# Kernel tuning notes

Measured on AMD Instinct MI355X. Metric: run time of the kernel, lower is better.

The kernel has to match this reference:

```python
import jax, jax.numpy as jnp
import numpy as np

S, D, H, KV, HD = 2048, 4096, 32, 8, 128
N_REP = H // KV
THETA = 50000.0
EPS = 1e-6

# Precompute RoPE tables (constant, matches precompute_freqs_cis sliced to seq_len)
_freqs = 1.0 / THETA ** (np.arange(0, HD, 2)[: HD // 2].astype(np.float32) / HD)
_ang = np.outer(np.arange(S), _freqs).astype(np.float32)  # [S, HD//2]
COS = jnp.asarray(np.cos(_ang))
SIN = jnp.asarray(np.sin(_ang))


def _rope(x):
    # x: [S, nh, HD]; treat last dim as HD//2 complex pairs, multiply by e^{i*ang}
    xr = x.astype(jnp.float32).reshape(S, x.shape[1], HD // 2, 2)
    x0, x1 = xr[..., 0], xr[..., 1]
    c = COS[:, None, :]
    s = SIN[:, None, :]
    o0 = x0 * c - x1 * s
    o1 = x0 * s + x1 * c
    return jnp.stack((o0, o1), axis=-1).reshape(S, x.shape[1], HD)


def setup_inputs() -> dict:
    key = jax.random.key(0)
    k1, k2, k3, k4, k5 = jax.random.split(key, 5)
    w_scale = 0.02
    return {
        "hidden": jax.random.normal(k1, (S, D), dtype=jnp.float32),
        "norm_w": jnp.ones((D,), dtype=jnp.float32),
        "wq": jax.random.normal(k2, (H * HD, D), dtype=jnp.float32) * w_scale,
        "wk": jax.random.normal(k3, (KV * HD, D), dtype=jnp.float32) * w_scale,
        "wv": jax.random.normal(k4, (KV * HD, D), dtype=jnp.float32) * w_scale,
        "wo": jax.random.normal(k5, (D, D), dtype=jnp.float32) * w_scale,
    }


def reference(hidden, norm_w, wq, wk, wv, wo):
    # RMSNorm (per token)
    x = hidden.astype(jnp.float32)
    h = x * jax.lax.rsqrt(jnp.mean(x * x, axis=-1, keepdims=True) + EPS) * norm_w

    # QKV projections (eqx.nn.Linear: y = W @ x, no bias)
    q = (h @ wq.T).reshape(S, H, HD)
    k = (h @ wk.T).reshape(S, KV, HD)
    v = (h @ wv.T).reshape(S, KV, HD)

    # RoPE in fp32 (apply_rotary_emb with dtype=float32)
    q = _rope(q)
    k = _rope(k)

    # GQA: repeat kv heads to match query heads
    k = jnp.repeat(k[:, :, None, :], N_REP, axis=2).reshape(S, H, HD)
    v = jnp.repeat(v[:, :, None, :], N_REP, axis=2).reshape(S, H, HD)

    # Causal attention (full score matrix + softmax, as in the original)
    scores = jnp.einsum("shd,thd->hst", q, k) / jnp.sqrt(jnp.float32(HD))
    mask = jnp.triu(jnp.full((S, S), float("-inf"), dtype=scores.dtype), k=1)
    probs = jax.nn.softmax(scores + mask, axis=-1)
    attn = jnp.einsum("hst,thd->shd", probs, v).reshape(S, H * HD)

    # Output projection
    return attn @ wo.T
```

## Files before the change

### kernel.cpp

```cpp
#include <hip/hip_runtime.h>
#include <stdint.h>
#include <stddef.h>

#define AS1 __attribute__((address_space(1)))
#define AS3 __attribute__((address_space(3)))

typedef short short8 __attribute__((ext_vector_type(8)));
typedef float v4f    __attribute__((ext_vector_type(4)));
typedef unsigned short us4 __attribute__((ext_vector_type(4)));

constexpr int S_  = 2048;
constexpr int D_  = 4096;
constexpr int H_  = 32;
constexpr int KV_ = 8;
constexpr int HD_ = 128;
constexpr int NQKV_ = H_*HD_ + 2*KV_*HD_;
constexpr float SCALE_L2E = 0.12751744154070513f;
constexpr float NLOG2T_64 = -0.24390063241307518f;

__device__ __forceinline__ unsigned short f2bf(float f){
  union { float f; unsigned u; } v; v.f = f;
  unsigned r = v.u + 0x7FFFu + ((v.u >> 16) & 1u);
  return (unsigned short)(r >> 16);
}
__device__ __forceinline__ float bf2f(unsigned short h){
  union { unsigned u; float f; } v; v.u = ((unsigned)h) << 16; return v.f;
}

__device__ __forceinline__ void gl_lds16(const unsigned short* g, unsigned short* l){
  __builtin_amdgcn_global_load_lds((AS1 unsigned int*)(uintptr_t)g,
                                   (AS3 unsigned int*)l, 16, 0, 0);
}

__global__ __launch_bounds__(256) void rmsnorm_k(const float* __restrict__ hidden,
                                                 const float* __restrict__ w,
                                                 unsigned short* __restrict__ out){
  const int s = blockIdx.x, tid = threadIdx.x;
  const float4* row = (const float4*)(hidden + (size_t)s * D_);
  float4 v[4];
  float ss = 0.f;
  #pragma unroll
  for (int i = 0; i < 4; i++){
    float4 t = row[tid + 256*i]; v[i] = t;
    ss += t.x*t.x + t.y*t.y + t.z*t.z + t.w*t.w;
  }
  #pragma unroll
  for (int off = 32; off >= 1; off >>= 1) ss += __shfl_xor(ss, off, 64);
  __shared__ float wsum[4];
  if ((tid & 63) == 0) wsum[tid >> 6] = ss;
  __syncthreads();
  const float total = wsum[0] + wsum[1] + wsum[2] + wsum[3];
  const float r = rsqrtf(total * (1.0f / D_) + 1e-6f);
  const float4* w4 = (const float4*)w;
  us4* o = (us4*)(out + (size_t)s * D_);
  #pragma unroll
  for (int i = 0; i < 4; i++){
    float4 t = v[i], ww = w4[tid + 256*i];
    us4 p;
    p[0] = f2bf(t.x * r * ww.x); p[1] = f2bf(t.y * r * ww.y);
    p[2] = f2bf(t.z * r * ww.z); p[3] = f2bf(t.w * r * ww.w);
    o[tid + 256*i] = p;
  }
}

__global__ __launch_bounds__(256) void cast_k(const float* __restrict__ src,
                                              unsigned short* __restrict__ dst, int n4){
  const int i = blockIdx.x * 256 + threadIdx.x;
  if (i >= n4) return;
  float4 t = ((const float4*)src)[i];
  us4 p;
  p[0] = f2bf(t.x); p[1] = f2bf(t.y); p[2] = f2bf(t.z); p[3] = f2bf(t.w);
  ((us4*)dst)[i] = p;
}

__global__ __launch_bounds__(256) void gemm_bt(const unsigned short* __restrict__ A,
                                               const unsigned short* __restrict__ B,
                                               void* __restrict__ Cp,
                                               int K, int ldc, int f32out){
  __shared__ __align__(16) unsigned short sA[128*32];
  __shared__ __align__(16) unsigned short sB[128*32];
  const int tid = threadIdx.x;
  const int wave = tid >> 6, lane = tid & 63, l15 = lane & 15, quad = lane >> 4;
  const int m0 = blockIdx.y * 128, n0 = blockIdx.x * 128;
  const int wm = wave & 1, wn = wave >> 1;

  v4f acc[4][4];
  #pragma unroll
  for (int i = 0; i < 4; i++)
    #pragma unroll
    for (int j = 0; j < 4; j++) acc[i][j] = (v4f){0.f,0.f,0.f,0.f};

  const int arow = tid >> 2, acol = (tid & 3) * 8;
  const unsigned short* gA = A + (size_t)(m0 + arow) * K + acol;
  const unsigned short* gB = B + (size_t)(n0 + arow) * K + acol;
  unsigned short* lA = sA + wave * 512;
  unsigned short* lB = sB + wave * 512;

  for (int kt = 0; kt < K; kt += 32){
    gl_lds16(gA,                 lA);
    gl_lds16(gA + (size_t)64*K,  lA + 2048);
    gl_lds16(gB,                 lB);
    gl_lds16(gB + (size_t)64*K,  lB + 2048);
    gA += 32; gB += 32;
    __syncthreads();

    short8 af[4], bfr[4];
    #pragma unroll
    for (int mt = 0; mt < 4; mt++)
      af[mt] = *(const short8*)(sA + (wm*64 + mt*16 + l15)*32 + quad*8);
    #pragma unroll
    for (int nt = 0; nt < 4; nt++)
      bfr[nt] = *(const short8*)(sB + (wn*64 + nt*16 + l15)*32 + quad*8);
    #pragma unroll
    for (int mt = 0; mt < 4; mt++)
      #pragma unroll
      for (int nt = 0; nt < 4; nt++)
        acc[mt][nt] = __builtin_amdgcn_mfma_f32_16x16x32_bf16(af[mt], bfr[nt], acc[mt][nt], 0, 0, 0);
    __syncthreads();
  }

  if (f32out){
    float* Cf = (float*)Cp;
    #pragma unroll
    for (int mt = 0; mt < 4; mt++)
      #pragma unroll
      for (int r = 0; r < 4; r++){
        const size_t row = (size_t)(m0 + wm*64 + mt*16 + quad*4 + r);
        float* crow = Cf + row * ldc + n0 + wn*64 + l15;
        #pragma unroll
        for (int nt = 0; nt < 4; nt++) crow[nt*16] = acc[mt][nt][r];
      }
  } else {
    unsigned short* Cb = (unsigned short*)Cp;
    #pragma unroll
    for (int mt = 0; mt < 4; mt++)
      #pragma unroll
      for (int r = 0; r < 4; r++){
        const size_t row = (size_t)(m0 + wm*64 + mt*16 + quad*4 + r);
        unsigned short* crow = Cb + row * ldc + n0 + wn*64 + l15;
        #pragma unroll
        for (int nt = 0; nt < 4; nt++) crow[nt*16] = f2bf(acc[mt][nt][r]);
      }
  }
}

__global__ __launch_bounds__(256) void rope_q_k(const unsigned short* __restrict__ qkv,
                                                unsigned short* __restrict__ qa){
  const int idx = blockIdx.x * 256 + threadIdx.x;
  const int j = idx & 63, h = (idx >> 6) & (H_-1), s = idx >> 11;
  const unsigned pair = *(const unsigned*)(qkv + (size_t)s*NQKV_ + h*HD_ + 2*j);
  const float x0 = bf2f((unsigned short)(pair & 0xffffu));
  const float x1 = bf2f((unsigned short)(pair >> 16));
  const float ang = (float)s * exp2f((float)j * NLOG2T_64);
  const float c = __cosf(ang), sn = __sinf(ang);
  const unsigned o = (unsigned)f2bf((x0*c - x1*sn) * SCALE_L2E)
                   | ((unsigned)f2bf((x0*sn + x1*c) * SCALE_L2E) << 16);
  *(unsigned*)(qa + ((size_t)h*S_ + s)*HD_ + 2*j) = o;
}

__global__ __launch_bounds__(256) void rope_kk(const unsigned short* __restrict__ qkv,
                                               unsigned short* __restrict__ ka){
  const int idx = blockIdx.x * 256 + threadIdx.x;
  const int j = idx & 63, kv = (idx >> 6) & (KV_-1), s = idx >> 9;
  const unsigned pair = *(const unsigned*)(qkv + (size_t)s*NQKV_ + H_*HD_ + kv*HD_ + 2*j);
  const float x0 = bf2f((unsigned short)(pair & 0xffffu));
  const float x1 = bf2f((unsigned short)(pair >> 16));
  const float ang = (float)s * exp2f((float)j * NLOG2T_64);
  const float c = __cosf(ang), sn = __sinf(ang);
  const unsigned o = (unsigned)f2bf(x0*c - x1*sn) | ((unsigned)f2bf(x0*sn + x1*c) << 16);
  *(unsigned*)(ka + ((size_t)kv*S_ + s)*HD_ + 2*j) = o;
}

__global__ __launch_bounds__(256) void vtrans_k(const unsigned short* __restrict__ qkv,
                                                unsigned short* __restrict__ vt){
  const int idx = blockIdx.x * 256 + threadIdx.x;
  const int s = idx & (S_-1), d = (idx >> 11) & (HD_-1), kv = idx >> 18;
  vt[idx] = qkv[(size_t)s*NQKV_ + (H_+KV_)*HD_ + kv*HD_ + d];
}

__device__ __forceinline__ void stage_kv(const unsigned short* __restrict__ ka,
                                         const unsigned short* __restrict__ vt,
                                         unsigned short* sKbuf, unsigned short* sVbuf,
                                         int hk, int t0, int wave, int lane){
  const int l15 = lane & 15, quad = lane >> 4;
  #pragma unroll
  for (int j = 0; j < 4; j++){
    const int c = wave*4 + j;
    const int kt = c >> 2, kk = c & 3;
    gl_lds16(ka + (size_t)(hk*S_ + t0 + kt*16 + l15)*HD_ + kk*32 + quad*8,
             sKbuf + c*512);
  }
  #pragma unroll
  for (int j = 0; j < 4; j++){
    const int c = wave*4 + j;
    const int nt = c >> 1, kk2 = c & 1;
    gl_lds16(vt + (size_t)(hk*HD_ + nt*16 + l15)*S_ + t0 + kk2*32 + quad*8,
             sVbuf + c*512);
  }
}

__global__ __launch_bounds__(256, 2) void attn_k(const unsigned short* __restrict__ qa,
                                                 const unsigned short* __restrict__ ka,
                                                 const unsigned short* __restrict__ vt,
                                                 unsigned short* __restrict__ out){
  const int h = blockIdx.x, p = blockIdx.y;
  const int tid = threadIdx.x, wave = tid >> 6, lane = tid & 63;
  const int l15 = lane & 15, quad = lane >> 4;
  const int hk = h >> 2;
  const int nbB = 32 - p;
  const int total = nbB + p + 1;

  __shared__ __align__(16) unsigned short sK[2][8192];
  __shared__ __align__(16) unsigned short sV[2][8192];
  __shared__ __align__(16) unsigned short sP[4][1024];
  unsigned short* pl = &sP[wave][0];

  short8 ones;
  #pragma unroll
  for (int i = 0; i < 8; i++) ones[i] = (short)0x3F80;

  int tile = 31 - p;
  short8 qf[4];
  {
    const unsigned short* qb = qa + (size_t)(h*S_ + tile*64 + wave*16 + l15)*HD_ + quad*8;
    #pragma unroll
    for (int kk = 0; kk < 4; kk++) qf[kk] = *(const short8*)(qb + kk*32);
  }

  v4f O[8];
  #pragma unroll
  for (int nt = 0; nt < 8; nt++) O[nt] = (v4f){0.f,0.f,0.f,0.f};
  float mrow[4], lrow[4];
  #pragma unroll
  for (int r = 0; r < 4; r++){ mrow[r] = -1e30f; lrow[r] = 0.f; }

  stage_kv(ka, vt, sK[0], sV[0], hk, 0, wave, lane);
  __syncthreads();

  for (int u = 0; u < total; ++u){
    const int cur = u & 1;
    if (u + 1 < total){
      const int b2 = (u + 1 < nbB) ? u + 1 : u + 1 - nbB;
      stage_kv(ka, vt, sK[cur^1], sV[cur^1], hk, b2*64, wave, lane);
    }

    const unsigned short* Kb = &sK[cur][0];
    v4f sc[4];
    #pragma unroll
    for (int kt = 0; kt < 4; kt++) sc[kt] = (v4f){0.f,0.f,0.f,0.f};
    #pragma unroll
    for (int kt = 0; kt < 4; kt++)
      #pragma unroll
      for (int kk = 0; kk < 4; kk++){
        const short8 kf = *(const short8*)(Kb + (kt*4 + kk)*512 + lane*8);
        sc[kt] = __builtin_amdgcn_mfma_f32_16x16x32_bf16(qf[kk], kf, sc[kt], 0, 0, 0);
      }

    const bool diag = (u == nbB - 1) || (u == total - 1);
    float alpha[4];
    #pragma unroll
    for (int r = 0; r < 4; r++){
      float a0 = sc[0][r], a1 = sc[1][r], a2 = sc[2][r], a3 = sc[3][r];
      if (diag){
        const int rloc = wave*16 + quad*4 + r;
        if (     l15 > rloc) a0 = -1e30f;
        if (16 + l15 > rloc) a1 = -1e30f;
        if (32 + l15 > rloc) a2 = -1e30f;
        if (48 + l15 > rloc) a3 = -1e30f;
      }
      float mx = fmaxf(fmaxf(a0, a1), fmaxf(a2, a3));
      #pragma unroll
      for (int off = 1; off < 16; off <<= 1) mx = fmaxf(mx, __shfl_xor(mx, off, 16));
      const float mnew = fmaxf(mrow[r], mx);
      alpha[r] = exp2f(mrow[r] - mnew);
      mrow[r] = mnew;
      const float e0 = exp2f(a0 - mnew);
      const float e1 = exp2f(a1 - mnew);
      const float e2 = exp2f(a2 - mnew);
      const float e3 = exp2f(a3 - mnew);
      const int mr = (quad*4 + r)*8 + (l15 & 7);
      const int hi = (l15 >> 3) * 128;
      pl[      hi       + mr] = f2bf(e0);
      pl[      hi + 256 + mr] = f2bf(e1);
      pl[512 + hi       + mr] = f2bf(e2);
      pl[512 + hi + 256 + mr] = f2bf(e3);
    }
    #pragma unroll
    for (int nt = 0; nt < 8; nt++)
      #pragma unroll
      for (int r = 0; r < 4; r++) O[nt][r] *= alpha[r];

    __builtin_amdgcn_s_waitcnt(0xC07F);
    const short8 pf0 = *(const short8*)(pl + lane*8);
    const short8 pf1 = *(const short8*)(pl + 512 + lane*8);

    v4f rs = (v4f){0.f,0.f,0.f,0.f};
    rs = __builtin_amdgcn_mfma_f32_16x16x32_bf16(pf0, ones, rs, 0, 0, 0);
    rs = __builtin_amdgcn_mfma_f32_16x16x32_bf16(pf1, ones, rs, 0, 0, 0);

    const unsigned short* Vb = &sV[cur][0];
    #pragma unroll
    for (int nt = 0; nt < 8; nt++){
      const short8 vf0 = *(const short8*)(Vb + (nt*2    )*512 + lane*8);
      const short8 vf1 = *(const short8*)(Vb + (nt*2 + 1)*512 + lane*8);
      O[nt] = __builtin_amdgcn_mfma_f32_16x16x32_bf16(pf0, vf0, O[nt], 0, 0, 0);
      O[nt] = __builtin_amdgcn_mfma_f32_16x16x32_bf16(pf1, vf1, O[nt], 0, 0, 0);
    }
    #pragma unroll
    for (int r = 0; r < 4; r++) lrow[r] = lrow[r]*alpha[r] + rs[r];

    __syncthreads();

    if (u == nbB - 1){
      #pragma unroll
      for (int r = 0; r < 4; r++){
        const float inv = 1.0f / lrow[r];
        const size_t row = (size_t)(tile*64 + wave*16 + quad*4 + r);
        #pragma unroll
        for (int nt = 0; nt < 8; nt++)
          out[row*D_ + h*HD_ + nt*16 + l15] = f2bf(O[nt][r] * inv);
      }
      tile = p;
      const unsigned short* qb = qa + (size_t)(h*S_ + tile*64 + wave*16 + l15)*HD_ + quad*8;
      #pragma unroll
      for (int kk = 0; kk < 4; kk++) qf[kk] = *(const short8*)(qb + kk*32);
      #pragma unroll
      for (int nt = 0; nt < 8; nt++) O[nt] = (v4f){0.f,0.f,0.f,0.f};
      #pragma unroll
      for (int r = 0; r < 4; r++){ mrow[r] = -1e30f; lrow[r] = 0.f; }
    }
  }

  #pragma unroll
  for (int r = 0; r < 4; r++){
    const float inv = 1.0f / lrow[r];
    const size_t row = (size_t)(tile*64 + wave*16 + quad*4 + r);
    #pragma unroll
    for (int nt = 0; nt < 8; nt++)
      out[row*D_ + h*HD_ + nt*16 + l15] = f2bf(O[nt][r] * inv);
  }
}

extern "C" void kernel_launch(void* const* d_in, const int* in_sizes, int n_in,
                              void* d_out, int out_size, void* d_ws, size_t ws_size,
                              hipStream_t stream){
  (void)in_sizes; (void)n_in; (void)out_size; (void)ws_size;
  const float* hidden = (const float*)d_in[0];
  const float* norm_w = (const float*)d_in[1];
  const float* wq = (const float*)d_in[2];
  const float* wk = (const float*)d_in[3];
  const float* wv = (const float*)d_in[4];
  const float* wo = (const float*)d_in[5];

  char* ws = (char*)d_ws;
  unsigned short* h_bf  = (unsigned short*)(ws);
  unsigned short* wqkv  = (unsigned short*)(ws + (size_t)(16u) * 1048576u);
  unsigned short* qkv   = (unsigned short*)(ws + (size_t)(64u) * 1048576u);
  unsigned short* qa    = (unsigned short*)(ws + (size_t)(88u) * 1048576u);
  unsigned short* ka    = (unsigned short*)(ws + (size_t)(104u) * 1048576u);
  unsigned short* vt    = (unsigned short*)(ws + (size_t)(108u) * 1048576u);
  unsigned short* wo_bf = (unsigned short*)(ws + (size_t)(16u) * 1048576u);
  unsigned short* attnb = (unsigned short*)(ws + (size_t)(48u) * 1048576u);

  rmsnorm_k<<<S_, 256, 0, stream>>>(hidden, norm_w, h_bf);

  cast_k<<<(D_*D_/4)/256, 256, 0, stream>>>(wq, wqkv, D_*D_/4);
  cast_k<<<(KV_*HD_*D_/4)/256, 256, 0, stream>>>(wk, wqkv + (size_t)H_*HD_*D_, KV_*HD_*D_/4);
  cast_k<<<(KV_*HD_*D_/4)/256, 256, 0, stream>>>(wv, wqkv + (size_t)(H_+KV_)*HD_*D_, KV_*HD_*D_/4);

  gemm_bt<<<dim3(NQKV_/128, S_/128), 256, 0, stream>>>(h_bf, wqkv, qkv, D_, NQKV_, 0);

  rope_q_k<<<(S_*H_*64)/256, 256, 0, stream>>>(qkv, qa);
  rope_kk <<<(S_*KV_*64)/256, 256, 0, stream>>>(qkv, ka);
  vtrans_k<<<(KV_*HD_*S_)/256, 256, 0, stream>>>(qkv, vt);

  cast_k<<<(D_*D_/4)/256, 256, 0, stream>>>(wo, wo_bf, D_*D_/4);

  attn_k<<<dim3(H_, 16), 256, 0, stream>>>(qa, ka, vt, attnb);

  gemm_bt<<<dim3(D_/128, S_/128), 256, 0, stream>>>(attnb, wo_bf, d_out, D_, D_, 1);
}
```

Measured before the change: 556.8 us.

## Fuse RoPE and V transpose into QKV GEMM epilogue, retile attention, split-K output GEMM

```diff
diff --git a/kernel.cpp b/kernel.cpp
--- a/kernel.cpp
+++ b/kernel.cpp
@@ -14,7 +14,6 @@
 constexpr int H_  = 32;
 constexpr int KV_ = 8;
 constexpr int HD_ = 128;
-constexpr int NQKV_ = H_*HD_ + 2*KV_*HD_;
 constexpr float SCALE_L2E = 0.12751744154070513f;
 constexpr float NLOG2T_64 = -0.24390063241307518f;
 
@@ -22,9 +21,6 @@
   union { float f; unsigned u; } v; v.f = f;
   unsigned r = v.u + 0x7FFFu + ((v.u >> 16) & 1u);
   return (unsigned short)(r >> 16);
-}
-__device__ __forceinline__ float bf2f(unsigned short h){
-  union { unsigned u; float f; } v; v.u = ((unsigned)h) << 16; return v.f;
 }
 
 __device__ __forceinline__ void gl_lds16(const unsigned short* g, unsigned short* l){
@@ -73,10 +69,11 @@
   ((us4*)dst)[i] = p;
 }
 
-__global__ __launch_bounds__(256) void gemm_bt(const unsigned short* __restrict__ A,
-                                               const unsigned short* __restrict__ B,
-                                               void* __restrict__ Cp,
-                                               int K, int ldc, int f32out){
+__global__ __launch_bounds__(256) void gemm_qkv(const unsigned short* __restrict__ A,
+                                                const unsigned short* __restrict__ B,
+                                                unsigned short* __restrict__ qa,
+                                                unsigned short* __restrict__ ka,
+                                                unsigned short* __restrict__ vt){
   __shared__ __align__(16) unsigned short sA[128*32];
   __shared__ __align__(16) unsigned short sB[128*32];
   const int tid = threadIdx.x;
@@ -91,16 +88,16 @@
     for (int j = 0; j < 4; j++) acc[i][j] = (v4f){0.f,0.f,0.f,0.f};
 
   const int arow = tid >> 2, acol = (tid & 3) * 8;
-  const unsigned short* gA = A + (size_t)(m0 + arow) * K + acol;
-  const unsigned short* gB = B + (size_t)(n0 + arow) * K + acol;
+  const unsigned short* gA = A + (size_t)(m0 + arow) * D_ + acol;
+  const unsigned short* gB = B + (size_t)(n0 + arow) * D_ + acol;
   unsigned short* lA = sA + wave * 512;
   unsigned short* lB = sB + wave * 512;
 
-  for (int kt = 0; kt < K; kt += 32){
+  for (int kt = 0; kt < D_; kt += 32){
     gl_lds16(gA,                 lA);
-    gl_lds16(gA + (size_t)64*K,  lA + 2048);
+    gl_lds16(gA + (size_t)64*D_, lA + 2048);
     gl_lds16(gB,                 lB);
-    gl_lds16(gB + (size_t)64*K,  lB + 2048);
+    gl_lds16(gB + (size_t)64*D_, lB + 2048);
     gA += 32; gB += 32;
     __syncthreads();
 
@@ -119,107 +116,153 @@
     __syncthreads();
   }
 
-  if (f32out){
-    float* Cf = (float*)Cp;
+  const int dloc0 = wn*64 + l15;
+  if (n0 < 5120){
+    float fr[4];
+    #pragma unroll
+    for (int nt = 0; nt < 4; nt++)
+      fr[nt] = exp2f((float)((dloc0 + nt*16) >> 1) * NLOG2T_64);
+    const bool isQ = (n0 < 4096);
+    unsigned short* base;
+    if (isQ) base = qa + (size_t)(n0 >> 7) * S_ * HD_;
+    else     base = ka + (size_t)((n0 - 4096) >> 7) * S_ * HD_;
     #pragma unroll
     for (int mt = 0; mt < 4; mt++)
       #pragma unroll
       for (int r = 0; r < 4; r++){
-        const size_t row = (size_t)(m0 + wm*64 + mt*16 + quad*4 + r);
-        float* crow = Cf + row * ldc + n0 + wn*64 + l15;
+        const int row = m0 + wm*64 + mt*16 + quad*4 + r;
         #pragma unroll
-        for (int nt = 0; nt < 4; nt++) crow[nt*16] = acc[mt][nt][r];
+        for (int nt = 0; nt < 4; nt++){
+          const float x = acc[mt][nt][r];
+          const float y = __shfl_xor(x, 1, 64);
+          const float ang = (float)row * fr[nt];
+          const float c = __cosf(ang), sn = __sinf(ang);
+          float o = (l15 & 1) ? (y*sn + x*c) : (x*c - y*sn);
+          if (isQ) o *= SCALE_L2E;
+          base[(size_t)row*HD_ + dloc0 + nt*16] = f2bf(o);
+        }
       }
   } else {
-    unsigned short* Cb = (unsigned short*)Cp;
+    unsigned short* vb = vt + (size_t)((n0 - 5120) >> 7) * HD_ * S_;
     #pragma unroll
     for (int mt = 0; mt < 4; mt++)
       #pragma unroll
       for (int r = 0; r < 4; r++){
-        const size_t row = (size_t)(m0 + wm*64 + mt*16 + quad*4 + r);
-        unsigned short* crow = Cb + row * ldc + n0 + wn*64 + l15;
+        const int row = m0 + wm*64 + mt*16 + quad*4 + r;
         #pragma unroll
-        for (int nt = 0; nt < 4; nt++) crow[nt*16] = f2bf(acc[mt][nt][r]);
+        for (int nt = 0; nt < 4; nt++)
+          vb[(size_t)(dloc0 + nt*16)*S_ + row] = f2bf(acc[mt][nt][r]);
       }
   }
 }
 
-__global__ __launch_bounds__(256) void rope_q_k(const unsigned short* __restrict__ qkv,
-                                                unsigned short* __restrict__ qa){
-  const int idx = blockIdx.x * 256 + threadIdx.x;
-  const int j = idx & 63, h = (idx >> 6) & (H_-1), s = idx >> 11;
-  const unsigned pair = *(const unsigned*)(qkv + (size_t)s*NQKV_ + h*HD_ + 2*j);
-  const float x0 = bf2f((unsigned short)(pair & 0xffffu));
-  const float x1 = bf2f((unsigned short)(pair >> 16));
-  const float ang = (float)s * exp2f((float)j * NLOG2T_64);
-  const float c = __cosf(ang), sn = __sinf(ang);
-  const unsigned o = (unsigned)f2bf((x0*c - x1*sn) * SCALE_L2E)
-                   | ((unsigned)f2bf((x0*sn + x1*c) * SCALE_L2E) << 16);
-  *(unsigned*)(qa + ((size_t)h*S_ + s)*HD_ + 2*j) = o;
-}
-
-__global__ __launch_bounds__(256) void rope_kk(const unsigned short* __restrict__ qkv,
-                                               unsigned short* __restrict__ ka){
-  const int idx = blockIdx.x * 256 + threadIdx.x;
-  const int j = idx & 63, kv = (idx >> 6) & (KV_-1), s = idx >> 9;
-  const unsigned pair = *(const unsigned*)(qkv + (size_t)s*NQKV_ + H_*HD_ + kv*HD_ + 2*j);
-  const float x0 = bf2f((unsigned short)(pair & 0xffffu));
-  const float x1 = bf2f((unsigned short)(pair >> 16));
-  const float ang = (float)s * exp2f((float)j * NLOG2T_64);
-  const float c = __cosf(ang), sn = __sinf(ang);
-  const unsigned o = (unsigned)f2bf(x0*c - x1*sn) | ((unsigned)f2bf(x0*sn + x1*c) << 16);
-  *(unsigned*)(ka + ((size_t)kv*S_ + s)*HD_ + 2*j) = o;
-}
-
-__global__ __launch_bounds__(256) void vtrans_k(const unsigned short* __restrict__ qkv,
-                                                unsigned short* __restrict__ vt){
-  const int idx = blockIdx.x * 256 + threadIdx.x;
-  const int s = idx & (S_-1), d = (idx >> 11) & (HD_-1), kv = idx >> 18;
-  vt[idx] = qkv[(size_t)s*NQKV_ + (H_+KV_)*HD_ + kv*HD_ + d];
-}
-
-__device__ __forceinline__ void stage_kv(const unsigned short* __restrict__ ka,
-                                         const unsigned short* __restrict__ vt,
-                                         unsigned short* sKbuf, unsigned short* sVbuf,
-                                         int hk, int t0, int wave, int lane){
+__global__ __launch_bounds__(256) void gemm_bt(const unsigned short* __restrict__ A,
+                                               const unsigned short* __restrict__ B,
+                                               float* __restrict__ Cp,
+                                               int lda, int klen, int ldc, size_t zstr){
+  __shared__ __align__(16) unsigned short sA[128*32];
+  __shared__ __align__(16) unsigned short sB[128*32];
+  const int tid = threadIdx.x;
+  const int wave = tid >> 6, lane = tid & 63, l15 = lane & 15, quad = lane >> 4;
+  const int m0 = blockIdx.y * 128, n0 = blockIdx.x * 128;
+  const int wm = wave & 1, wn = wave >> 1;
+  const int koff = blockIdx.z * klen;
+
+  v4f acc[4][4];
+  #pragma unroll
+  for (int i = 0; i < 4; i++)
+    #pragma unroll
+    for (int j = 0; j < 4; j++) acc[i][j] = (v4f){0.f,0.f,0.f,0.f};
+
+  const int arow = tid >> 2, acol = (tid & 3) * 8;
+  const unsigned short* gA = A + (size_t)(m0 + arow) * lda + koff + acol;
+  const unsigned short* gB = B + (size_t)(n0 + arow) * lda + koff + acol;
+  unsigned short* lA = sA + wave * 512;
+  unsigned short* lB = sB + wave * 512;
+
+  for (int kt = 0; kt < klen; kt += 32){
+    gl_lds16(gA,                  lA);
+    gl_lds16(gA + (size_t)64*lda, lA + 2048);
+    gl_lds16(gB,                  lB);
+    gl_lds16(gB + (size_t)64*lda, lB + 2048);
+    gA += 32; gB += 32;
+    __syncthreads();
+
+    short8 af[4], bfr[4];
+    #pragma unroll
+    for (int mt = 0; mt < 4; mt++)
+      af[mt] = *(const short8*)(sA + (wm*64 + mt*16 + l15)*32 + quad*8);
+    #pragma unroll
+    for (int nt = 0; nt < 4; nt++)
+      bfr[nt] = *(const short8*)(sB + (wn*64 + nt*16 + l15)*32 + quad*8);
+    #pragma unroll
+    for (int mt = 0; mt < 4; mt++)
+      #pragma unroll
+      for (int nt = 0; nt < 4; nt++)
+        acc[mt][nt] = __builtin_amdgcn_mfma_f32_16x16x32_bf16(af[mt], bfr[nt], acc[mt][nt], 0, 0, 0);
+    __syncthreads();
+  }
+
+  float* Cf = Cp + (size_t)blockIdx.z * zstr;
+  #pragma unroll
+  for (int mt = 0; mt < 4; mt++)
+    #pragma unroll
+    for (int r = 0; r < 4; r++){
+      const size_t row = (size_t)(m0 + wm*64 + mt*16 + quad*4 + r);
+      float* crow = Cf + row * ldc + n0 + wn*64 + l15;
+      #pragma unroll
+      for (int nt = 0; nt < 4; nt++) crow[nt*16] = acc[mt][nt][r];
+    }
+}
+
+__global__ __launch_bounds__(256) void add2_k(const float4* __restrict__ a,
+                                              const float4* __restrict__ b,
+                                              float4* __restrict__ o, int n4){
+  const int i = blockIdx.x * 256 + threadIdx.x;
+  if (i >= n4) return;
+  float4 x = a[i], y = b[i];
+  o[i] = make_float4(x.x+y.x, x.y+y.y, x.z+y.z, x.w+y.w);
+}
+
+__device__ __forceinline__ void stage32(const unsigned short* __restrict__ ka,
+                                        const unsigned short* __restrict__ vt,
+                                        unsigned short* sKb, unsigned short* sVb,
+                                        int hk, int t0, int wave, int lane){
   const int l15 = lane & 15, quad = lane >> 4;
   #pragma unroll
-  for (int j = 0; j < 4; j++){
-    const int c = wave*4 + j;
+  for (int j = 0; j < 2; j++){
+    const int c = wave*2 + j;
     const int kt = c >> 2, kk = c & 3;
     gl_lds16(ka + (size_t)(hk*S_ + t0 + kt*16 + l15)*HD_ + kk*32 + quad*8,
-             sKbuf + c*512);
-  }
-  #pragma unroll
-  for (int j = 0; j < 4; j++){
-    const int c = wave*4 + j;
-    const int nt = c >> 1, kk2 = c & 1;
-    gl_lds16(vt + (size_t)(hk*HD_ + nt*16 + l15)*S_ + t0 + kk2*32 + quad*8,
-             sVbuf + c*512);
-  }
-}
-
-__global__ __launch_bounds__(256, 2) void attn_k(const unsigned short* __restrict__ qa,
+             sKb + c*512);
+  }
+  #pragma unroll
+  for (int j = 0; j < 2; j++){
+    const int c = wave*2 + j;
+    gl_lds16(vt + (size_t)(hk*HD_ + c*16 + l15)*S_ + t0 + quad*8,
+             sVb + c*512);
+  }
+}
+
+__global__ __launch_bounds__(256, 4) void attn_k(const unsigned short* __restrict__ qa,
                                                  const unsigned short* __restrict__ ka,
                                                  const unsigned short* __restrict__ vt,
                                                  unsigned short* __restrict__ out){
-  const int h = blockIdx.x, p = blockIdx.y;
+  const int h = blockIdx.x, tile = 31 - (int)blockIdx.y;
   const int tid = threadIdx.x, wave = tid >> 6, lane = tid & 63;
   const int l15 = lane & 15, quad = lane >> 4;
   const int hk = h >> 2;
-  const int nbB = 32 - p;
-  const int total = nbB + p + 1;
-
-  __shared__ __align__(16) unsigned short sK[2][8192];
-  __shared__ __align__(16) unsigned short sV[2][8192];
-  __shared__ __align__(16) unsigned short sP[4][1024];
+  const int nU = 2*tile + 2;
+
+  __shared__ __align__(16) unsigned short sK[2][4096];
+  __shared__ __align__(16) unsigned short sV[2][4096];
+  __shared__ __align__(16) unsigned short sP[4][512];
   unsigned short* pl = &sP[wave][0];
 
   short8 ones;
   #pragma unroll
   for (int i = 0; i < 8; i++) ones[i] = (short)0x3F80;
 
-  int tile = 31 - p;
   short8 qf[4];
   {
     const unsigned short* qb = qa + (size_t)(h*S_ + tile*64 + wave*16 + l15)*HD_ + quad*8;
@@ -234,41 +277,38 @@
   #pragma unroll
   for (int r = 0; r < 4; r++){ mrow[r] = -1e30f; lrow[r] = 0.f; }
 
-  stage_kv(ka, vt, sK[0], sV[0], hk, 0, wave, lane);
+  stage32(ka, vt, sK[0], sV[0], hk, 0, wave, lane);
   __syncthreads();
 
-  for (int u = 0; u < total; ++u){
+  const int rowlo = tile*64 + wave*16;
+
+  for (int u = 0; u < nU; ++u){
     const int cur = u & 1;
-    if (u + 1 < total){
-      const int b2 = (u + 1 < nbB) ? u + 1 : u + 1 - nbB;
-      stage_kv(ka, vt, sK[cur^1], sV[cur^1], hk, b2*64, wave, lane);
+    if (u + 1 < nU)
+      stage32(ka, vt, sK[cur^1], sV[cur^1], hk, (u+1)*32, wave, lane);
+    const int t0 = u * 32;
+
+    const unsigned short* Kb = &sK[cur][0];
+    v4f sc0 = (v4f){0.f,0.f,0.f,0.f}, sc1 = (v4f){0.f,0.f,0.f,0.f};
+    #pragma unroll
+    for (int kk = 0; kk < 4; kk++){
+      const short8 kf0 = *(const short8*)(Kb + kk*512 + lane*8);
+      const short8 kf1 = *(const short8*)(Kb + (4 + kk)*512 + lane*8);
+      sc0 = __builtin_amdgcn_mfma_f32_16x16x32_bf16(qf[kk], kf0, sc0, 0, 0, 0);
+      sc1 = __builtin_amdgcn_mfma_f32_16x16x32_bf16(qf[kk], kf1, sc1, 0, 0, 0);
     }
 
-    const unsigned short* Kb = &sK[cur][0];
-    v4f sc[4];
-    #pragma unroll
-    for (int kt = 0; kt < 4; kt++) sc[kt] = (v4f){0.f,0.f,0.f,0.f};
-    #pragma unroll
-    for (int kt = 0; kt < 4; kt++)
-      #pragma unroll
-      for (int kk = 0; kk < 4; kk++){
-        const short8 kf = *(const short8*)(Kb + (kt*4 + kk)*512 + lane*8);
-        sc[kt] = __builtin_amdgcn_mfma_f32_16x16x32_bf16(qf[kk], kf, sc[kt], 0, 0, 0);
+    const bool diag = (t0 + 31 > rowlo);
+    float alpha[4];
+    #pragma unroll
+    for (int r = 0; r < 4; r++){
+      float a0 = sc0[r], a1 = sc1[r];
+      if (diag){
+        const int row = rowlo + quad*4 + r;
+        if (t0      + l15 > row) a0 = -1e30f;
+        if (t0 + 16 + l15 > row) a1 = -1e30f;
       }
-
-    const bool diag = (u == nbB - 1) || (u == total - 1);
-    float alpha[4];
-    #pragma unroll
-    for (int r = 0; r < 4; r++){
-      float a0 = sc[0][r], a1 = sc[1][r], a2 = sc[2][r], a3 = sc[3][r];
-      if (diag){
-        const int rloc = wave*16 + quad*4 + r;
-        if (     l15 > rloc) a0 = -1e30f;
-        if (16 + l15 > rloc) a1 = -1e30f;
-        if (32 + l15 > rloc) a2 = -1e30f;
-        if (48 + l15 > rloc) a3 = -1e30f;
-      }
-      float mx = fmaxf(fmaxf(a0, a1), fmaxf(a2, a3));
+      float mx = fmaxf(a0, a1);
       #pragma unroll
       for (int off = 1; off < 16; off <<= 1) mx = fmaxf(mx, __shfl_xor(mx, off, 16));
       const float mnew = fmaxf(mrow[r], mx);
@@ -276,14 +316,10 @@
       mrow[r] = mnew;
       const float e0 = exp2f(a0 - mnew);
       const float e1 = exp2f(a1 - mnew);
-      const float e2 = exp2f(a2 - mnew);
-      const float e3 = exp2f(a3 - mnew);
       const int mr = (quad*4 + r)*8 + (l15 & 7);
       const int hi = (l15 >> 3) * 128;
-      pl[      hi       + mr] = f2bf(e0);
-      pl[      hi + 256 + mr] = f2bf(e1);
-      pl[512 + hi       + mr] = f2bf(e2);
-      pl[512 + hi + 256 + mr] = f2bf(e3);
+      pl[      hi + mr] = f2bf(e0);
+      pl[256 + hi + mr] = f2bf(e1);
     }
     #pragma unroll
     for (int nt = 0; nt < 8; nt++)
@@ -291,44 +327,21 @@
       for (int r = 0; r < 4; r++) O[nt][r] *= alpha[r];
 
     __builtin_amdgcn_s_waitcnt(0xC07F);
-    const short8 pf0 = *(const short8*)(pl + lane*8);
-    const short8 pf1 = *(const short8*)(pl + 512 + lane*8);
+    const short8 pf = *(const short8*)(pl + lane*8);
 
     v4f rs = (v4f){0.f,0.f,0.f,0.f};
-    rs = __builtin_amdgcn_mfma_f32_16x16x32_bf16(pf0, ones, rs, 0, 0, 0);
-    rs = __builtin_amdgcn_mfma_f32_16x16x32_bf16(pf1, ones, rs, 0, 0, 0);
+    rs = __builtin_amdgcn_mfma_f32_16x16x32_bf16(pf, ones, rs, 0, 0, 0);
 
     const unsigned short* Vb = &sV[cur][0];
     #pragma unroll
     for (int nt = 0; nt < 8; nt++){
-      const short8 vf0 = *(const short8*)(Vb + (nt*2    )*512 + lane*8);
-      const short8 vf1 = *(const short8*)(Vb + (nt*2 + 1)*512 + lane*8);
-      O[nt] = __builtin_amdgcn_mfma_f32_16x16x32_bf16(pf0, vf0, O[nt], 0, 0, 0);
-      O[nt] = __builtin_amdgcn_mfma_f32_16x16x32_bf16(pf1, vf1, O[nt], 0, 0, 0);
+      const short8 vf = *(const short8*)(Vb + nt*512 + lane*8);
+      O[nt] = __builtin_amdgcn_mfma_f32_16x16x32_bf16(pf, vf, O[nt], 0, 0, 0);
     }
     #pragma unroll
     for (int r = 0; r < 4; r++) lrow[r] = lrow[r]*alpha[r] + rs[r];
 
     __syncthreads();
-
-    if (u == nbB - 1){
-      #pragma unroll
-      for (int r = 0; r < 4; r++){
-        const float inv = 1.0f / lrow[r];
-        const size_t row = (size_t)(tile*64 + wave*16 + quad*4 + r);
-        #pragma unroll
-        for (int nt = 0; nt < 8; nt++)
-          out[row*D_ + h*HD_ + nt*16 + l15] = f2bf(O[nt][r] * inv);
-      }
-      tile = p;
-      const unsigned short* qb = qa + (size_t)(h*S_ + tile*64 + wave*16 + l15)*HD_ + quad*8;
-      #pragma unroll
-      for (int kk = 0; kk < 4; kk++) qf[kk] = *(const short8*)(qb + kk*32);
-      #pragma unroll
-      for (int nt = 0; nt < 8; nt++) O[nt] = (v4f){0.f,0.f,0.f,0.f};
-      #pragma unroll
-      for (int r = 0; r < 4; r++){ mrow[r] = -1e30f; lrow[r] = 0.f; }
-    }
   }
 
   #pragma unroll
@@ -344,7 +357,7 @@
 extern "C" void kernel_launch(void* const* d_in, const int* in_sizes, int n_in,
                               void* d_out, int out_size, void* d_ws, size_t ws_size,
                               hipStream_t stream){
-  (void)in_sizes; (void)n_in; (void)out_size; (void)ws_size;
+  (void)in_sizes; (void)n_in; (void)out_size;
   const float* hidden = (const float*)d_in[0];
   const float* norm_w = (const float*)d_in[1];
   const float* wq = (const float*)d_in[2];
@@ -354,13 +367,13 @@
 
   char* ws = (char*)d_ws;
   unsigned short* h_bf  = (unsigned short*)(ws);
-  unsigned short* wqkv  = (unsigned short*)(ws + (size_t)(16u) * 1048576u);
-  unsigned short* qkv   = (unsigned short*)(ws + (size_t)(64u) * 1048576u);
-  unsigned short* qa    = (unsigned short*)(ws + (size_t)(88u) * 1048576u);
-  unsigned short* ka    = (unsigned short*)(ws + (size_t)(104u) * 1048576u);
-  unsigned short* vt    = (unsigned short*)(ws + (size_t)(108u) * 1048576u);
-  unsigned short* wo_bf = (unsigned short*)(ws + (size_t)(16u) * 1048576u);
-  unsigned short* attnb = (unsigned short*)(ws + (size_t)(48u) * 1048576u);
+  unsigned short* wqkv  = (unsigned short*)(ws + (size_t)16 * 1048576u);
+  unsigned short* qa    = (unsigned short*)(ws + (size_t)64 * 1048576u);
+  unsigned short* ka    = (unsigned short*)(ws + (size_t)80 * 1048576u);
+  unsigned short* vt    = (unsigned short*)(ws + (size_t)84 * 1048576u);
+  unsigned short* wo_bf = (unsigned short*)(ws + (size_t)16 * 1048576u);
+  unsigned short* attnb = (unsigned short*)(ws + (size_t)48 * 1048576u);
+  float*          part  = (float*)        (ws + (size_t)88 * 1048576u);
 
   rmsnorm_k<<<S_, 256, 0, stream>>>(hidden, norm_w, h_bf);
 
@@ -368,15 +381,20 @@
   cast_k<<<(KV_*HD_*D_/4)/256, 256, 0, stream>>>(wk, wqkv + (size_t)H_*HD_*D_, KV_*HD_*D_/4);
   cast_k<<<(KV_*HD_*D_/4)/256, 256, 0, stream>>>(wv, wqkv + (size_t)(H_+KV_)*HD_*D_, KV_*HD_*D_/4);
 
-  gemm_bt<<<dim3(NQKV_/128, S_/128), 256, 0, stream>>>(h_bf, wqkv, qkv, D_, NQKV_, 0);
-
-  rope_q_k<<<(S_*H_*64)/256, 256, 0, stream>>>(qkv, qa);
-  rope_kk <<<(S_*KV_*64)/256, 256, 0, stream>>>(qkv, ka);
-  vtrans_k<<<(KV_*HD_*S_)/256, 256, 0, stream>>>(qkv, vt);
+  gemm_qkv<<<dim3(48, 16), 256, 0, stream>>>(h_bf, wqkv, qa, ka, vt);
 
   cast_k<<<(D_*D_/4)/256, 256, 0, stream>>>(wo, wo_bf, D_*D_/4);
 
-  attn_k<<<dim3(H_, 16), 256, 0, stream>>>(qa, ka, vt, attnb);
-
-  gemm_bt<<<dim3(D_/128, S_/128), 256, 0, stream>>>(attnb, wo_bf, d_out, D_, D_, 1);
-}
+  attn_k<<<dim3(H_, 32), 256, 0, stream>>>(qa, ka, vt, attnb);
+
+  if (ws_size >= (size_t)152 * 1048576u){
+    gemm_bt<<<dim3(D_/128, S_/128, 2), 256, 0, stream>>>(attnb, wo_bf, part,
+                                                         D_, D_/2, D_, (size_t)S_*D_);
+    add2_k<<<(S_*D_/4)/256, 256, 0, stream>>>((const float4*)part,
+                                              (const float4*)(part + (size_t)S_*D_),
+                                              (float4*)d_out, S_*D_/4);
+  } else {
+    gemm_bt<<<dim3(D_/128, S_/128), 256, 0, stream>>>(attnb, wo_bf, (float*)d_out,
+                                                      D_, D_, D_, 0);
+  }
+}
```

Measured after the change: 611.0 us. 9.7% more time.
